# Kernel optimization log

Measured on AMD Instinct MI355X. Metric: run time of the kernel, lower is better.

Reference implementation:

```python
import jax, jax.numpy as jnp
import numpy as np

N = 80000        # nodes
E = 1280000      # edges (avg degree 16)
D_IN, H1, H2, D_OUT = 64, 64, 64, 64


def _glorot(key, fan_in, fan_out):
    s = np.sqrt(6.0 / (fan_in + fan_out)).astype(np.float32)
    return jax.random.uniform(key, (fan_in, fan_out), jnp.float32, -s, s)


def setup_inputs() -> dict:
    key = jax.random.key(0)
    ks = jax.random.split(key, 5)
    X = jax.random.normal(ks[0], (N, D_IN), jnp.float32)
    edge_index = jax.random.randint(ks[1], (2, E), 0, N, dtype=jnp.int32).astype(jnp.int64)
    W1 = _glorot(ks[2], D_IN, H1)
    W2 = _glorot(ks[3], H1, H2)
    W3 = _glorot(ks[4], H2, D_OUT)
    b1 = jnp.zeros((H1,), jnp.float32)
    b2 = jnp.zeros((H2,), jnp.float32)
    b3 = jnp.zeros((D_OUT,), jnp.float32)
    return {"X": X, "edge_index": edge_index,
            "W1": W1, "b1": b1, "W2": W2, "b2": b2, "W3": W3, "b3": b3}


def _gcn_conv(x, W, b, src, dst, n):
    """PyG GCNConv: symmetric-normalized mean over A + I, then linear + bias.
    x' = D^{-1/2} (A + I) D^{-1/2} (x W) + b, deg counts self-loops."""
    x = x @ W                                   # [N, F_out]
    # in-degree including self loop (edge weights are 1)
    deg = jnp.ones((n,), x.dtype).at[dst].add(1.0)
    dinv = jax.lax.rsqrt(deg)                   # deg >= 1 always
    coef = dinv[src] * dinv[dst]                # [E]
    msg = x[src] * coef[:, None]                # [E, F_out] gather
    agg = jnp.zeros_like(x).at[dst].add(msg)    # scatter-add to targets
    agg = agg + x * (dinv * dinv)[:, None]      # self-loop contribution
    return agg + b


def reference(X, edge_index, W1, b1, W2, b2, W3, b3):
    src, dst = edge_index[0], edge_index[1]
    n = X.shape[0]
    h = jax.nn.relu(_gcn_conv(X, W1, b1, src, dst, n))
    h = jax.nn.relu(_gcn_conv(h, W2, b2, src, dst, n))
    out = _gcn_conv(h, W3, b3, src, dst, n)     # no activation on last layer
    return out
```

## Files before the change

### kernel.cpp

```cpp
#include <hip/hip_runtime.h>
#include <hip/hip_fp16.h>

#define NN 80000
#define NE 1280000
#define F  64
#define BSH 9
#define NB  157
#define CAP 12288
#define EPB 5120
#define EPT 10
#define PBLK (NE / EPB)

typedef _Float16 half_t;
typedef _Float16 half8 __attribute__((ext_vector_type(8)));
typedef float f32x4 __attribute__((ext_vector_type(4)));
typedef unsigned int uint_t;

__device__ __forceinline__ float2 h2f2(uint_t u) {
    __half2 h = *(__half2*)&u;
    return __half22float2(h);
}

__device__ __forceinline__ int ld_src(const int* __restrict__ idx, int e, int is64) {
    return is64 ? idx[2 * e] : idx[e];
}
__device__ __forceinline__ int ld_dst(const int* __restrict__ idx, int e, int is64) {
    return is64 ? idx[2 * NE + 2 * e] : idx[NE + e];
}

__global__ __launch_bounds__(512) void partition_kernel(
        const int* __restrict__ idx,
        int* __restrict__ bcur, int* __restrict__ ebuf) {
    __shared__ int cnt[NB];
    __shared__ int lbase[NB];
    __shared__ int gbase[NB];
    __shared__ int lds_val[EPB];
    __shared__ int lds_gaddr[EPB];
    __shared__ int is64_s;
    int tid = threadIdx.x;
    if (tid == 0) is64_s = 1;
    if (tid < NB) cnt[tid] = 0;
    __syncthreads();
    if (idx[2 * tid + 1] != 0) is64_s = 0;
    __syncthreads();
    int is64 = is64_s;
    int e0 = blockIdx.x * EPB;
    int val[EPT], br[EPT];
    #pragma unroll
    for (int j = 0; j < EPT; ++j) {
        int e = e0 + j * 512 + tid;
        int s = ld_src(idx, e, is64);
        int d = ld_dst(idx, e, is64);
        int b = d >> BSH;
        val[j] = ((d & ((1 << BSH) - 1)) << 17) | s;
        int r = atomicAdd(&cnt[b], 1);
        br[j] = (b << 13) | r;
    }
    __syncthreads();
    if (tid < 64) {
        int carry = 0;
        for (int base = 0; base < NB; base += 64) {
            int i2 = base + tid;
            int v = (i2 < NB) ? cnt[i2] : 0;
            int incl = v;
            #pragma unroll
            for (int d2 = 1; d2 < 64; d2 <<= 1) {
                int t = __shfl_up(incl, d2, 64);
                if (tid >= d2) incl += t;
            }
            if (i2 < NB) lbase[i2] = carry + incl - v;
            carry += __shfl(incl, 63);
        }
    } else if (tid - 64 < NB) {
        int b = tid - 64;
        gbase[b] = atomicAdd(&bcur[b], cnt[b]);
    }
    __syncthreads();
    #pragma unroll
    for (int j = 0; j < EPT; ++j) {
        int b = br[j] >> 13, r = br[j] & 8191;
        int slot = lbase[b] + r;
        int g = gbase[b] + r;
        lds_val[slot]   = val[j];
        lds_gaddr[slot] = (g < CAP) ? (b * CAP + g) : -1;
    }
    __syncthreads();
    for (int i = tid; i < EPB; i += 512) {
        int a = lds_gaddr[i];
        if (a >= 0) ebuf[a] = lds_val[i];
    }
}

__global__ __launch_bounds__(1024) void bucket_sort_kernel(
        const int* __restrict__ bcur, const int* __restrict__ ebuf,
        int* __restrict__ edata, int* __restrict__ row_ptr,
        float* __restrict__ dinv) {
    __shared__ int cnt[512];
    __shared__ int off[512];
    __shared__ int lds_out[CAP];
    __shared__ int ebase_s;
    int b = blockIdx.x, tid = threadIdx.x;
    if (tid < 512) cnt[tid] = 0;
    if (tid < 64) {
        int carry = 0;
        for (int base = 0; base < NB; base += 64) {
            int i2 = base + tid;
            int v = (i2 < NB) ? min(bcur[i2], CAP) : 0;
            int incl = v;
            #pragma unroll
            for (int d2 = 1; d2 < 64; d2 <<= 1) {
                int t = __shfl_up(incl, d2, 64);
                if (tid >= d2) incl += t;
            }
            if (i2 == b) ebase_s = carry + incl - v;
            carry += __shfl(incl, 63);
        }
    }
    __syncthreads();
    int bcnt = min(bcur[b], CAP);
    int ebase = ebase_s;
    const int* src = ebuf + b * CAP;
    for (int i = tid; i < bcnt; i += 1024)
        atomicAdd(&cnt[src[i] >> 17], 1);
    __syncthreads();
    if (tid < 64) {
        int carry = 0;
        #pragma unroll
        for (int base = 0; base < 512; base += 64) {
            int v = cnt[base + tid];
            int incl = v;
            #pragma unroll
            for (int d2 = 1; d2 < 64; d2 <<= 1) {
                int t = __shfl_up(incl, d2, 64);
                if (tid >= d2) incl += t;
            }
            off[base + tid] = carry + incl - v;
            carry += __shfl(incl, 63);
        }
    }
    __syncthreads();
    int n0 = b << BSH;
    if (tid < 512) {
        int n = n0 + tid;
        if (n < NN) {
            row_ptr[n] = ebase + off[tid];
            dinv[n] = rsqrtf((float)cnt[tid] + 1.f);
        } else if (n == NN) {
            row_ptr[NN] = ebase + off[tid];
        }
    }
    __syncthreads();
    for (int i = tid; i < bcnt; i += 1024) {
        int w = src[i];
        int pos = atomicAdd(&off[w >> 17], 1);
        lds_out[pos] = w & 0x1FFFF;
    }
    __syncthreads();
    for (int i = tid; i < bcnt; i += 1024)
        edata[ebase + i] = lds_out[i];
}

__global__ void prescale_kernel(const float* __restrict__ x, const float* __restrict__ dinv,
                                half_t* __restrict__ y) {
    int tid = blockIdx.x * blockDim.x + threadIdx.x;
    if (tid >= NN * 16) return;
    int n = tid >> 4, q = tid & 15;
    float c = dinv[n];
    float4 v = ((const float4*)(x + (size_t)n * F))[q];
    half_t h[4] = { (half_t)(v.x * c), (half_t)(v.y * c),
                    (half_t)(v.z * c), (half_t)(v.w * c) };
    ((uint2*)(y + (size_t)n * F))[q] = *(uint2*)h;
}

__global__ __launch_bounds__(256) void gather_kernel(const half_t* __restrict__ y,
        const int* __restrict__ edata, const int* __restrict__ row_ptr,
        half_t* __restrict__ agg) {
    int n = blockIdx.x * 4 + (threadIdx.x >> 6);
    int lane = threadIdx.x & 63;
    int sub = lane >> 3;
    int fl  = lane & 7;
    int p0 = row_ptr[n], p1 = row_ptr[n + 1];
    uint4 us = ((const uint4*)(y + (size_t)n * F))[fl];
    float a[8];
    #pragma unroll
    for (int i = 0; i < 8; ++i) a[i] = 0.f;
    int p = p0;
    while (p + 32 <= p1) {
        int s[4];
        #pragma unroll
        for (int j = 0; j < 4; ++j) s[j] = edata[p + j * 8 + sub];
        uint4 u[4];
        #pragma unroll
        for (int j = 0; j < 4; ++j)
            u[j] = ((const uint4*)(y + (size_t)s[j] * F))[fl];
        #pragma unroll
        for (int j = 0; j < 4; ++j) {
            float2 f0 = h2f2(u[j].x), f1 = h2f2(u[j].y);
            float2 f2 = h2f2(u[j].z), f3 = h2f2(u[j].w);
            a[0] += f0.x; a[1] += f0.y; a[2] += f1.x; a[3] += f1.y;
            a[4] += f2.x; a[5] += f2.y; a[6] += f3.x; a[7] += f3.y;
        }
        p += 32;
    }
    int rem = p1 - p;
    if (rem > 0) {
        int s[4]; float m[4];
        #pragma unroll
        for (int j = 0; j < 4; ++j) {
            int q = p + j * 8 + sub;
            s[j] = edata[q < p1 ? q : p1 - 1];
            m[j] = (q < p1) ? 1.f : 0.f;
        }
        uint4 u[4];
        u[0] = ((const uint4*)(y + (size_t)s[0] * F))[fl];
        if (rem > 8)  u[1] = ((const uint4*)(y + (size_t)s[1] * F))[fl];
        if (rem > 16) u[2] = ((const uint4*)(y + (size_t)s[2] * F))[fl];
        if (rem > 24) u[3] = ((const uint4*)(y + (size_t)s[3] * F))[fl];
        {
            float2 f0 = h2f2(u[0].x), f1 = h2f2(u[0].y);
            float2 f2 = h2f2(u[0].z), f3 = h2f2(u[0].w);
            a[0] = fmaf(m[0], f0.x, a[0]); a[1] = fmaf(m[0], f0.y, a[1]);
            a[2] = fmaf(m[0], f1.x, a[2]); a[3] = fmaf(m[0], f1.y, a[3]);
            a[4] = fmaf(m[0], f2.x, a[4]); a[5] = fmaf(m[0], f2.y, a[5]);
            a[6] = fmaf(m[0], f3.x, a[6]); a[7] = fmaf(m[0], f3.y, a[7]);
        }
        if (rem > 8) {
            float2 f0 = h2f2(u[1].x), f1 = h2f2(u[1].y);
            float2 f2 = h2f2(u[1].z), f3 = h2f2(u[1].w);
            a[0] = fmaf(m[1], f0.x, a[0]); a[1] = fmaf(m[1], f0.y, a[1]);
            a[2] = fmaf(m[1], f1.x, a[2]); a[3] = fmaf(m[1], f1.y, a[3]);
            a[4] = fmaf(m[1], f2.x, a[4]); a[5] = fmaf(m[1], f2.y, a[5]);
            a[6] = fmaf(m[1], f3.x, a[6]); a[7] = fmaf(m[1], f3.y, a[7]);
        }
        if (rem > 16) {
            float2 f0 = h2f2(u[2].x), f1 = h2f2(u[2].y);
            float2 f2 = h2f2(u[2].z), f3 = h2f2(u[2].w);
            a[0] = fmaf(m[2], f0.x, a[0]); a[1] = fmaf(m[2], f0.y, a[1]);
            a[2] = fmaf(m[2], f1.x, a[2]); a[3] = fmaf(m[2], f1.y, a[3]);
            a[4] = fmaf(m[2], f2.x, a[4]); a[5] = fmaf(m[2], f2.y, a[5]);
            a[6] = fmaf(m[2], f3.x, a[6]); a[7] = fmaf(m[2], f3.y, a[7]);
        }
        if (rem > 24) {
            float2 f0 = h2f2(u[3].x), f1 = h2f2(u[3].y);
            float2 f2 = h2f2(u[3].z), f3 = h2f2(u[3].w);
            a[0] = fmaf(m[3], f0.x, a[0]); a[1] = fmaf(m[3], f0.y, a[1]);
            a[2] = fmaf(m[3], f1.x, a[2]); a[3] = fmaf(m[3], f1.y, a[3]);
            a[4] = fmaf(m[3], f2.x, a[4]); a[5] = fmaf(m[3], f2.y, a[5]);
            a[6] = fmaf(m[3], f3.x, a[6]); a[7] = fmaf(m[3], f3.y, a[7]);
        }
    }
    #pragma unroll
    for (int i = 0; i < 8; ++i) {
        a[i] += __shfl_down(a[i], 32);
        a[i] += __shfl_down(a[i], 16);
        a[i] += __shfl_down(a[i], 8);
    }
    if (sub == 0) {
        float dv = rsqrtf((float)(p1 - p0) + 1.f);
        float2 s0 = h2f2(us.x), s1 = h2f2(us.y), s2 = h2f2(us.z), s3 = h2f2(us.w);
        half_t h[8] = {
            (half_t)(dv * (a[0] + s0.x)), (half_t)(dv * (a[1] + s0.y)),
            (half_t)(dv * (a[2] + s1.x)), (half_t)(dv * (a[3] + s1.y)),
            (half_t)(dv * (a[4] + s2.x)), (half_t)(dv * (a[5] + s2.y)),
            (half_t)(dv * (a[6] + s3.x)), (half_t)(dv * (a[7] + s3.y)) };
        ((uint4*)(agg + (size_t)n * F))[fl] = *(uint4*)h;
    }
}

template <int RELU, int SCALE, int LAST>
__global__ __launch_bounds__(256) void gemm_mfma(
        const half_t* __restrict__ A, const float* __restrict__ W,
        const float* __restrict__ bias, const float* __restrict__ dinv,
        half_t* __restrict__ out_h, float* __restrict__ out_f32) {
    __shared__ half_t Wt[64][72];
    __shared__ half_t xt[128][72];
    int tid = threadIdx.x;
    for (int i = tid; i < 4096; i += 256) {
        int k = i >> 6, n2 = i & 63;
        Wt[n2][k] = (half_t)W[i];
    }
    int n0 = blockIdx.x * 128;
    for (int i2 = tid; i2 < 2048; i2 += 256) {
        int r = i2 >> 4, c = i2 & 15;
        ((uint2*)&xt[r][0])[c] = ((const uint2*)(A + (size_t)(n0 + r) * F))[c];
    }
    __syncthreads();
    int wv = tid >> 6, lane = tid & 63;
    int m = lane & 15, q = lane >> 4;
    #pragma unroll
    for (int rt = 0; rt < 2; ++rt) {
        int rbase = wv * 32 + rt * 16;
        const half_t* arow = &xt[rbase + m][q * 8];
        half8 A0 = *(const half8*)arow;
        half8 A1 = *(const half8*)(arow + 32);
        #pragma unroll
        for (int ct = 0; ct < 4; ++ct) {
            const half_t* brow = &Wt[ct * 16 + m][q * 8];
            half8 B0 = *(const half8*)brow;
            half8 B1 = *(const half8*)(brow + 32);
            f32x4 c = {0.f, 0.f, 0.f, 0.f};
            c = __builtin_amdgcn_mfma_f32_16x16x32_f16(A0, B0, c, 0, 0, 0);
            c = __builtin_amdgcn_mfma_f32_16x16x32_f16(A1, B1, c, 0, 0, 0);
            float bv = bias[ct * 16 + m];
            #pragma unroll
            for (int r = 0; r < 4; ++r) {
                int row = n0 + rbase + q * 4 + r;
                float v = c[r] + bv;
                if (RELU) v = fmaxf(v, 0.f);
                if (SCALE) v *= dinv[row];
                int col = ct * 16 + m;
                if (LAST) out_f32[(size_t)row * F + col] = v;
                else      out_h[(size_t)row * F + col] = (half_t)v;
            }
        }
    }
}

extern "C" void kernel_launch(void* const* d_in, const int* in_sizes, int n_in,
                              void* d_out, int out_size, void* d_ws, size_t ws_size,
                              hipStream_t stream) {
    const float* X  = (const float*)d_in[0];
    const int*  idx = (const int*)d_in[1];
    const float* W1 = (const float*)d_in[2];
    const float* b1 = (const float*)d_in[3];
    const float* W2 = (const float*)d_in[4];
    const float* b2 = (const float*)d_in[5];
    const float* W3 = (const float*)d_in[6];
    const float* b3 = (const float*)d_in[7];
    float* out = (float*)d_out;

    char* ws = (char*)d_ws;
    int*    bcur    = (int*)(ws + 256);
    int*    row_ptr = (int*)(ws + 1024);
    float*  dinv    = (float*)(ws + 321280);
    int*    edata   = (int*)(ws + 641536);
    half_t* ybufA   = (half_t*)(ws + 5761536);
    half_t* ybufB   = (half_t*)(ws + 16001536);
    int*    ebuf    = (int*)(ws + 26241536);

    hipMemsetAsync(bcur, 0, NB * sizeof(int), stream);
    partition_kernel<<<PBLK, 512, 0, stream>>>(idx, bcur, ebuf);
    bucket_sort_kernel<<<NB, 1024, 0, stream>>>(bcur, ebuf, edata, row_ptr, dinv);
    prescale_kernel<<<(NN * 16) / 256, 256, 0, stream>>>(X, dinv, ybufA);

    const int gBlocks = NN / 4;
    const int mBlocks = NN / 128;

    gather_kernel<<<gBlocks, 256, 0, stream>>>(ybufA, edata, row_ptr, ybufB);
    gemm_mfma<1, 1, 0><<<mBlocks, 256, 0, stream>>>(ybufB, W1, b1, dinv, ybufA, nullptr);
    gather_kernel<<<gBlocks, 256, 0, stream>>>(ybufA, edata, row_ptr, ybufB);
    gemm_mfma<1, 1, 0><<<mBlocks, 256, 0, stream>>>(ybufB, W2, b2, dinv, ybufA, nullptr);
    gather_kernel<<<gBlocks, 256, 0, stream>>>(ybufA, edata, row_ptr, ybufB);
    gemm_mfma<0, 0, 1><<<mBlocks, 256, 0, stream>>>(ybufB, W3, b3, dinv, nullptr, out);
}
```

Measured before the change: 228.7 us.

## Fuse gather aggregation with MFMA linear layer and fold prescale into bucket sort

```diff
diff --git a/kernel.cpp b/kernel.cpp
--- a/kernel.cpp
+++ b/kernel.cpp
@@ -93,8 +93,9 @@
 
 __global__ __launch_bounds__(1024) void bucket_sort_kernel(
         const int* __restrict__ bcur, const int* __restrict__ ebuf,
+        const float* __restrict__ X,
         int* __restrict__ edata, int* __restrict__ row_ptr,
-        float* __restrict__ dinv) {
+        float* __restrict__ dinv, half_t* __restrict__ y0) {
     __shared__ int cnt[512];
     __shared__ int off[512];
     __shared__ int lds_out[CAP];
@@ -158,160 +159,159 @@
     __syncthreads();
     for (int i = tid; i < bcnt; i += 1024)
         edata[ebase + i] = lds_out[i];
-}
-
-__global__ void prescale_kernel(const float* __restrict__ x, const float* __restrict__ dinv,
-                                half_t* __restrict__ y) {
-    int tid = blockIdx.x * blockDim.x + threadIdx.x;
-    if (tid >= NN * 16) return;
-    int n = tid >> 4, q = tid & 15;
-    float c = dinv[n];
-    float4 v = ((const float4*)(x + (size_t)n * F))[q];
-    half_t h[4] = { (half_t)(v.x * c), (half_t)(v.y * c),
-                    (half_t)(v.z * c), (half_t)(v.w * c) };
-    ((uint2*)(y + (size_t)n * F))[q] = *(uint2*)h;
-}
-
-__global__ __launch_bounds__(256) void gather_kernel(const half_t* __restrict__ y,
+    for (int i = tid; i < (512 << 4); i += 1024) {
+        int r = i >> 4, qq = i & 15;
+        int n = n0 + r;
+        if (n < NN) {
+            float c = rsqrtf((float)cnt[r] + 1.f);
+            float4 v = ((const float4*)(X + (size_t)n * F))[qq];
+            half_t h[4] = { (half_t)(v.x * c), (half_t)(v.y * c),
+                            (half_t)(v.z * c), (half_t)(v.w * c) };
+            ((uint2*)(y0 + (size_t)n * F))[qq] = *(uint2*)h;
+        }
+    }
+}
+
+template <int RELU, int LAST>
+__global__ __launch_bounds__(512, 4) void fused_layer(
+        const half_t* __restrict__ y,
         const int* __restrict__ edata, const int* __restrict__ row_ptr,
-        half_t* __restrict__ agg) {
-    int n = blockIdx.x * 4 + (threadIdx.x >> 6);
-    int lane = threadIdx.x & 63;
+        const float* __restrict__ dinv,
+        const float* __restrict__ W, const float* __restrict__ bias,
+        half_t* __restrict__ out_h, float* __restrict__ out_f32) {
+    __shared__ __align__(16) half_t Wt[64][72];
+    __shared__ __align__(16) half_t xt[64][72];
+    int tid = threadIdx.x;
+    for (int i = tid; i < 4096; i += 512) {
+        int k = i >> 6, n2 = i & 63;
+        Wt[n2][k] = (half_t)W[i];
+    }
+    int wv = tid >> 6, lane = tid & 63;
     int sub = lane >> 3;
     int fl  = lane & 7;
-    int p0 = row_ptr[n], p1 = row_ptr[n + 1];
-    uint4 us = ((const uint4*)(y + (size_t)n * F))[fl];
-    float a[8];
+    int n0 = blockIdx.x * 64;
+    int rbase = wv * 8;
+    int rp = row_ptr[n0 + rbase + (lane < 9 ? lane : 8)];
+    #pragma unroll 1
+    for (int i = 0; i < 8; ++i) {
+        int n = n0 + rbase + i;
+        int p0 = __shfl(rp, i), p1 = __shfl(rp, i + 1);
+        uint4 us = ((const uint4*)(y + (size_t)n * F))[fl];
+        float a[8];
+        #pragma unroll
+        for (int j = 0; j < 8; ++j) a[j] = 0.f;
+        int p = p0;
+        while (p + 32 <= p1) {
+            int s[4];
+            #pragma unroll
+            for (int j = 0; j < 4; ++j) s[j] = edata[p + j * 8 + sub];
+            uint4 u[4];
+            #pragma unroll
+            for (int j = 0; j < 4; ++j)
+                u[j] = ((const uint4*)(y + (size_t)s[j] * F))[fl];
+            #pragma unroll
+            for (int j = 0; j < 4; ++j) {
+                float2 f0 = h2f2(u[j].x), f1 = h2f2(u[j].y);
+                float2 f2 = h2f2(u[j].z), f3 = h2f2(u[j].w);
+                a[0] += f0.x; a[1] += f0.y; a[2] += f1.x; a[3] += f1.y;
+                a[4] += f2.x; a[5] += f2.y; a[6] += f3.x; a[7] += f3.y;
+            }
+            p += 32;
+        }
+        int rem = p1 - p;
+        if (rem > 0) {
+            int s[4]; float m[4];
+            #pragma unroll
+            for (int j = 0; j < 4; ++j) {
+                int q = p + j * 8 + sub;
+                s[j] = edata[q < p1 ? q : p1 - 1];
+                m[j] = (q < p1) ? 1.f : 0.f;
+            }
+            uint4 u[4];
+            u[0] = ((const uint4*)(y + (size_t)s[0] * F))[fl];
+            if (rem > 8)  u[1] = ((const uint4*)(y + (size_t)s[1] * F))[fl];
+            if (rem > 16) u[2] = ((const uint4*)(y + (size_t)s[2] * F))[fl];
+            if (rem > 24) u[3] = ((const uint4*)(y + (size_t)s[3] * F))[fl];
+            {
+                float2 f0 = h2f2(u[0].x), f1 = h2f2(u[0].y);
+                float2 f2 = h2f2(u[0].z), f3 = h2f2(u[0].w);
+                a[0] = fmaf(m[0], f0.x, a[0]); a[1] = fmaf(m[0], f0.y, a[1]);
+                a[2] = fmaf(m[0], f1.x, a[2]); a[3] = fmaf(m[0], f1.y, a[3]);
+                a[4] = fmaf(m[0], f2.x, a[4]); a[5] = fmaf(m[0], f2.y, a[5]);
+                a[6] = fmaf(m[0], f3.x, a[6]); a[7] = fmaf(m[0], f3.y, a[7]);
+            }
+            if (rem > 8) {
+                float2 f0 = h2f2(u[1].x), f1 = h2f2(u[1].y);
+                float2 f2 = h2f2(u[1].z), f3 = h2f2(u[1].w);
+                a[0] = fmaf(m[1], f0.x, a[0]); a[1] = fmaf(m[1], f0.y, a[1]);
+                a[2] = fmaf(m[1], f1.x, a[2]); a[3] = fmaf(m[1], f1.y, a[3]);
+                a[4] = fmaf(m[1], f2.x, a[4]); a[5] = fmaf(m[1], f2.y, a[5]);
+                a[6] = fmaf(m[1], f3.x, a[6]); a[7] = fmaf(m[1], f3.y, a[7]);
+            }
+            if (rem > 16) {
+                float2 f0 = h2f2(u[2].x), f1 = h2f2(u[2].y);
+                float2 f2 = h2f2(u[2].z), f3 = h2f2(u[2].w);
+                a[0] = fmaf(m[2], f0.x, a[0]); a[1] = fmaf(m[2], f0.y, a[1]);
+                a[2] = fmaf(m[2], f1.x, a[2]); a[3] = fmaf(m[2], f1.y, a[3]);
+                a[4] = fmaf(m[2], f2.x, a[4]); a[5] = fmaf(m[2], f2.y, a[5]);
+                a[6] = fmaf(m[2], f3.x, a[6]); a[7] = fmaf(m[2], f3.y, a[7]);
+            }
+            if (rem > 24) {
+                float2 f0 = h2f2(u[3].x), f1 = h2f2(u[3].y);
+                float2 f2 = h2f2(u[3].z), f3 = h2f2(u[3].w);
+                a[0] = fmaf(m[3], f0.x, a[0]); a[1] = fmaf(m[3], f0.y, a[1]);
+                a[2] = fmaf(m[3], f1.x, a[2]); a[3] = fmaf(m[3], f1.y, a[3]);
+                a[4] = fmaf(m[3], f2.x, a[4]); a[5] = fmaf(m[3], f2.y, a[5]);
+                a[6] = fmaf(m[3], f3.x, a[6]); a[7] = fmaf(m[3], f3.y, a[7]);
+            }
+        }
+        #pragma unroll
+        for (int j = 0; j < 8; ++j) {
+            a[j] += __shfl_down(a[j], 32);
+            a[j] += __shfl_down(a[j], 16);
+            a[j] += __shfl_down(a[j], 8);
+        }
+        if (sub == 0) {
+            float dv = rsqrtf((float)(p1 - p0) + 1.f);
+            float2 s0 = h2f2(us.x), s1 = h2f2(us.y), s2 = h2f2(us.z), s3 = h2f2(us.w);
+            half_t h[8] = {
+                (half_t)(dv * (a[0] + s0.x)), (half_t)(dv * (a[1] + s0.y)),
+                (half_t)(dv * (a[2] + s1.x)), (half_t)(dv * (a[3] + s1.y)),
+                (half_t)(dv * (a[4] + s2.x)), (half_t)(dv * (a[5] + s2.y)),
+                (half_t)(dv * (a[6] + s3.x)), (half_t)(dv * (a[7] + s3.y)) };
+            *(uint4*)&xt[rbase + i][fl * 8] = *(uint4*)h;
+        }
+    }
+    __syncthreads();
+    int m = lane & 15, q = lane >> 4;
+    int rt = (wv & 3) * 16;
+    int ct0 = (wv >> 2) * 2;
+    const half_t* arow = &xt[rt + m][q * 8];
+    half8 A0 = *(const half8*)arow;
+    half8 A1 = *(const half8*)(arow + 32);
+    float dvr[4];
+    if (!LAST) {
+        #pragma unroll
+        for (int r = 0; r < 4; ++r) dvr[r] = dinv[n0 + rt + q * 4 + r];
+    }
     #pragma unroll
-    for (int i = 0; i < 8; ++i) a[i] = 0.f;
-    int p = p0;
-    while (p + 32 <= p1) {
-        int s[4];
-        #pragma unroll
-        for (int j = 0; j < 4; ++j) s[j] = edata[p + j * 8 + sub];
-        uint4 u[4];
-        #pragma unroll
-        for (int j = 0; j < 4; ++j)
-            u[j] = ((const uint4*)(y + (size_t)s[j] * F))[fl];
-        #pragma unroll
-        for (int j = 0; j < 4; ++j) {
-            float2 f0 = h2f2(u[j].x), f1 = h2f2(u[j].y);
-            float2 f2 = h2f2(u[j].z), f3 = h2f2(u[j].w);
-            a[0] += f0.x; a[1] += f0.y; a[2] += f1.x; a[3] += f1.y;
-            a[4] += f2.x; a[5] += f2.y; a[6] += f3.x; a[7] += f3.y;
-        }
-        p += 32;
-    }
-    int rem = p1 - p;
-    if (rem > 0) {
-        int s[4]; float m[4];
-        #pragma unroll
-        for (int j = 0; j < 4; ++j) {
-            int q = p + j * 8 + sub;
-            s[j] = edata[q < p1 ? q : p1 - 1];
-            m[j] = (q < p1) ? 1.f : 0.f;
-        }
-        uint4 u[4];
-        u[0] = ((const uint4*)(y + (size_t)s[0] * F))[fl];
-        if (rem > 8)  u[1] = ((const uint4*)(y + (size_t)s[1] * F))[fl];
-        if (rem > 16) u[2] = ((const uint4*)(y + (size_t)s[2] * F))[fl];
-        if (rem > 24) u[3] = ((const uint4*)(y + (size_t)s[3] * F))[fl];
-        {
-            float2 f0 = h2f2(u[0].x), f1 = h2f2(u[0].y);
-            float2 f2 = h2f2(u[0].z), f3 = h2f2(u[0].w);
-            a[0] = fmaf(m[0], f0.x, a[0]); a[1] = fmaf(m[0], f0.y, a[1]);
-            a[2] = fmaf(m[0], f1.x, a[2]); a[3] = fmaf(m[0], f1.y, a[3]);
-            a[4] = fmaf(m[0], f2.x, a[4]); a[5] = fmaf(m[0], f2.y, a[5]);
-            a[6] = fmaf(m[0], f3.x, a[6]); a[7] = fmaf(m[0], f3.y, a[7]);
-        }
-        if (rem > 8) {
-            float2 f0 = h2f2(u[1].x), f1 = h2f2(u[1].y);
-            float2 f2 = h2f2(u[1].z), f3 = h2f2(u[1].w);
-            a[0] = fmaf(m[1], f0.x, a[0]); a[1] = fmaf(m[1], f0.y, a[1]);
-            a[2] = fmaf(m[1], f1.x, a[2]); a[3] = fmaf(m[1], f1.y, a[3]);
-            a[4] = fmaf(m[1], f2.x, a[4]); a[5] = fmaf(m[1], f2.y, a[5]);
-            a[6] = fmaf(m[1], f3.x, a[6]); a[7] = fmaf(m[1], f3.y, a[7]);
-        }
-        if (rem > 16) {
-            float2 f0 = h2f2(u[2].x), f1 = h2f2(u[2].y);
-            float2 f2 = h2f2(u[2].z), f3 = h2f2(u[2].w);
-            a[0] = fmaf(m[2], f0.x, a[0]); a[1] = fmaf(m[2], f0.y, a[1]);
-            a[2] = fmaf(m[2], f1.x, a[2]); a[3] = fmaf(m[2], f1.y, a[3]);
-            a[4] = fmaf(m[2], f2.x, a[4]); a[5] = fmaf(m[2], f2.y, a[5]);
-            a[6] = fmaf(m[2], f3.x, a[6]); a[7] = fmaf(m[2], f3.y, a[7]);
-        }
-        if (rem > 24) {
-            float2 f0 = h2f2(u[3].x), f1 = h2f2(u[3].y);
-            float2 f2 = h2f2(u[3].z), f3 = h2f2(u[3].w);
-            a[0] = fmaf(m[3], f0.x, a[0]); a[1] = fmaf(m[3], f0.y, a[1]);
-            a[2] = fmaf(m[3], f1.x, a[2]); a[3] = fmaf(m[3], f1.y, a[3]);
-            a[4] = fmaf(m[3], f2.x, a[4]); a[5] = fmaf(m[3], f2.y, a[5]);
-            a[6] = fmaf(m[3], f3.x, a[6]); a[7] = fmaf(m[3], f3.y, a[7]);
-        }
-    }
-    #pragma unroll
-    for (int i = 0; i < 8; ++i) {
-        a[i] += __shfl_down(a[i], 32);
-        a[i] += __shfl_down(a[i], 16);
-        a[i] += __shfl_down(a[i], 8);
-    }
-    if (sub == 0) {
-        float dv = rsqrtf((float)(p1 - p0) + 1.f);
-        float2 s0 = h2f2(us.x), s1 = h2f2(us.y), s2 = h2f2(us.z), s3 = h2f2(us.w);
-        half_t h[8] = {
-            (half_t)(dv * (a[0] + s0.x)), (half_t)(dv * (a[1] + s0.y)),
-            (half_t)(dv * (a[2] + s1.x)), (half_t)(dv * (a[3] + s1.y)),
-            (half_t)(dv * (a[4] + s2.x)), (half_t)(dv * (a[5] + s2.y)),
-            (half_t)(dv * (a[6] + s3.x)), (half_t)(dv * (a[7] + s3.y)) };
-        ((uint4*)(agg + (size_t)n * F))[fl] = *(uint4*)h;
-    }
-}
-
-template <int RELU, int SCALE, int LAST>
-__global__ __launch_bounds__(256) void gemm_mfma(
-        const half_t* __restrict__ A, const float* __restrict__ W,
-        const float* __restrict__ bias, const float* __restrict__ dinv,
-        half_t* __restrict__ out_h, float* __restrict__ out_f32) {
-    __shared__ half_t Wt[64][72];
-    __shared__ half_t xt[128][72];
-    int tid = threadIdx.x;
-    for (int i = tid; i < 4096; i += 256) {
-        int k = i >> 6, n2 = i & 63;
-        Wt[n2][k] = (half_t)W[i];
-    }
-    int n0 = blockIdx.x * 128;
-    for (int i2 = tid; i2 < 2048; i2 += 256) {
-        int r = i2 >> 4, c = i2 & 15;
-        ((uint2*)&xt[r][0])[c] = ((const uint2*)(A + (size_t)(n0 + r) * F))[c];
-    }
-    __syncthreads();
-    int wv = tid >> 6, lane = tid & 63;
-    int m = lane & 15, q = lane >> 4;
-    #pragma unroll
-    for (int rt = 0; rt < 2; ++rt) {
-        int rbase = wv * 32 + rt * 16;
-        const half_t* arow = &xt[rbase + m][q * 8];
-        half8 A0 = *(const half8*)arow;
-        half8 A1 = *(const half8*)(arow + 32);
-        #pragma unroll
-        for (int ct = 0; ct < 4; ++ct) {
-            const half_t* brow = &Wt[ct * 16 + m][q * 8];
-            half8 B0 = *(const half8*)brow;
-            half8 B1 = *(const half8*)(brow + 32);
-            f32x4 c = {0.f, 0.f, 0.f, 0.f};
-            c = __builtin_amdgcn_mfma_f32_16x16x32_f16(A0, B0, c, 0, 0, 0);
-            c = __builtin_amdgcn_mfma_f32_16x16x32_f16(A1, B1, c, 0, 0, 0);
-            float bv = bias[ct * 16 + m];
-            #pragma unroll
-            for (int r = 0; r < 4; ++r) {
-                int row = n0 + rbase + q * 4 + r;
-                float v = c[r] + bv;
-                if (RELU) v = fmaxf(v, 0.f);
-                if (SCALE) v *= dinv[row];
-                int col = ct * 16 + m;
-                if (LAST) out_f32[(size_t)row * F + col] = v;
-                else      out_h[(size_t)row * F + col] = (half_t)v;
-            }
+    for (int c2 = 0; c2 < 2; ++c2) {
+        int ct = (ct0 + c2) * 16;
+        const half_t* brow = &Wt[ct + m][q * 8];
+        half8 B0 = *(const half8*)brow;
+        half8 B1 = *(const half8*)(brow + 32);
+        f32x4 c = {0.f, 0.f, 0.f, 0.f};
+        c = __builtin_amdgcn_mfma_f32_16x16x32_f16(A0, B0, c, 0, 0, 0);
+        c = __builtin_amdgcn_mfma_f32_16x16x32_f16(A1, B1, c, 0, 0, 0);
+        float bv = bias[ct + m];
+        #pragma unroll
+        for (int r = 0; r < 4; ++r) {
+            int row = n0 + rt + q * 4 + r;
+            float v = c[r] + bv;
+            if (RELU) v = fmaxf(v, 0.f);
+            int col = ct + m;
+            if (LAST) out_f32[(size_t)row * F + col] = v;
+            else      out_h[(size_t)row * F + col] = (half_t)(v * dvr[r]);
         }
     }
 }
@@ -340,16 +340,11 @@
 
     hipMemsetAsync(bcur, 0, NB * sizeof(int), stream);
     partition_kernel<<<PBLK, 512, 0, stream>>>(idx, bcur, ebuf);
-    bucket_sort_kernel<<<NB, 1024, 0, stream>>>(bcur, ebuf, edata, row_ptr, dinv);
-    prescale_kernel<<<(NN * 16) / 256, 256, 0, stream>>>(X, dinv, ybufA);
-
-    const int gBlocks = NN / 4;
-    const int mBlocks = NN / 128;
-
-    gather_kernel<<<gBlocks, 256, 0, stream>>>(ybufA, edata, row_ptr, ybufB);
-    gemm_mfma<1, 1, 0><<<mBlocks, 256, 0, stream>>>(ybufB, W1, b1, dinv, ybufA, nullptr);
-    gather_kernel<<<gBlocks, 256, 0, stream>>>(ybufA, edata, row_ptr, ybufB);
-    gemm_mfma<1, 1, 0><<<mBlocks, 256, 0, stream>>>(ybufB, W2, b2, dinv, ybufA, nullptr);
-    gather_kernel<<<gBlocks, 256, 0, stream>>>(ybufA, edata, row_ptr, ybufB);
-    gemm_mfma<0, 0, 1><<<mBlocks, 256, 0, stream>>>(ybufB, W3, b3, dinv, nullptr, out);
-}
+    bucket_sort_kernel<<<NB, 1024, 0, stream>>>(bcur, ebuf, X, edata, row_ptr, dinv, ybufA);
+
+    const int fBlocks = NN / 64;
+
+    fused_layer<1, 0><<<fBlocks, 512, 0, stream>>>(ybufA, edata, row_ptr, dinv, W1, b1, ybufB, nullptr);
+    fused_layer<1, 0><<<fBlocks, 512, 0, stream>>>(ybufB, edata, row_ptr, dinv, W2, b2, ybufA, nullptr);
+    fused_layer<0, 1><<<fBlocks, 512, 0, stream>>>(ybufA, edata, row_ptr, dinv, W3, b3, nullptr, out);
+}
```

Measured after the change: 221.5 us. 3.1% less time.
